# Kernel tuning notes

Measured on AMD Instinct MI355X. Metric: run time of the kernel, lower is better.

## Reference

```python
import jax, jax.numpy as jnp
import numpy as np

EPS = 1e-5

def conv2d(x, w, b=None, pad=1):
    # x: [B,C,H,W], w: [O,I,kh,kw]
    y = jax.lax.conv_general_dilated(x, w, (1, 1), [(pad, pad), (pad, pad)],
                                     dimension_numbers=('NCHW', 'OIHW', 'NCHW'))
    if b is not None:
        y = y + b[None, :, None, None]
    return y

def bn(x, g, b, m, v):
    # inference-mode batchnorm
    inv = g / jnp.sqrt(v + EPS)
    return x * inv[None, :, None, None] + (b - m * inv)[None, :, None, None]

def coord_conv(x, w, b):
    B, C, H, W = x.shape
    yy = jnp.broadcast_to(jnp.linspace(-1.0, 1.0, H)[:, None], (H, W))
    xx = jnp.broadcast_to(jnp.linspace(-1.0, 1.0, W)[None, :], (H, W))
    coords = jnp.broadcast_to(jnp.stack([xx, yy])[None], (B, 2, H, W)).astype(x.dtype)
    return conv2d(jnp.concatenate([x, coords], axis=1), w, b, pad=1)

def deform_conv(x, offset, w):
    # deformable conv v1, 3x3, pad=1, stride=1, no bias
    B, C, H, W = x.shape
    K = 9
    # offset channels interleaved (y, x) per kernel tap
    off = offset.reshape(B, K, 2, H, W)
    off_y, off_x = off[:, :, 0], off[:, :, 1]          # [B,9,H,W]
    k = jnp.arange(K)
    ko_y = (k // 3 - 1).astype(x.dtype)[None, :, None, None]
    ko_x = (k % 3 - 1).astype(x.dtype)[None, :, None, None]
    base_y = jnp.arange(H, dtype=x.dtype)[None, None, :, None]
    base_x = jnp.arange(W, dtype=x.dtype)[None, None, None, :]
    py = base_y + ko_y + off_y                          # [B,9,H,W]
    px = base_x + ko_x + off_x
    xf = x.reshape(B, C, H * W)
    y0 = jnp.floor(py)
    x0 = jnp.floor(px)
    acc = jnp.zeros((B, C, K, H, W), x.dtype)
    for dy in (0.0, 1.0):
        for dx in (0.0, 1.0):
            yy = y0 + dy
            xx = x0 + dx
            wgt = (1.0 - jnp.abs(py - yy)) * (1.0 - jnp.abs(px - xx))
            valid = (yy >= 0) & (yy < H) & (xx >= 0) & (xx < W)
            wgt = jnp.where(valid, wgt, 0.0)            # zero padding OOB
            yi = jnp.clip(yy, 0, H - 1).astype(jnp.int32)
            xi = jnp.clip(xx, 0, W - 1).astype(jnp.int32)
            idx = (yi * W + xi).reshape(B, K * H * W)
            v = jnp.take_along_axis(xf, idx[:, None, :], axis=2).reshape(B, C, K, H, W)
            acc = acc + v * wgt[:, None]
    wk = w.reshape(w.shape[0], w.shape[1], K)           # [O,I,9]
    return jnp.einsum('bckhw,ock->bohw', acc, wk)

def setup_inputs() -> dict:
    key = jax.random.key(0)
    ks = jax.random.split(key, 16)
    d_model, hd = 256, 64
    B, H, W = 8, 96, 96
    f32 = jnp.float32
    def bn_params(k):
        k1, k2, k3 = jax.random.split(k, 3)
        return (1.0 + 0.1 * jax.random.normal(k1, (hd,), f32),
                0.1 * jax.random.normal(k2, (hd,), f32),
                0.1 * jax.random.normal(k3, (hd,), f32),
                0.5 + jax.random.uniform(jax.random.fold_in(k, 7), (hd,), f32))
    bn1 = bn_params(ks[1]); bn2 = bn_params(ks[2]); bn3 = bn_params(ks[3]); bn4 = bn_params(ks[4])
    inp = {
        'features': jax.random.normal(ks[0], (B, H, W, d_model), f32),
        'coord_w': 0.05 * jax.random.normal(ks[5], (hd, d_model + 2, 3, 3), f32),
        'coord_b': jnp.zeros((hd,), f32),
        'bn1_g': bn1[0], 'bn1_b': bn1[1], 'bn1_m': bn1[2], 'bn1_v': bn1[3],
        'off_w': 0.01 * jax.random.normal(ks[6], (18, hd, 3, 3), f32),
        'off_b': 0.01 * jax.random.normal(ks[7], (18,), f32),
        'dc_w': 0.05 * jax.random.normal(ks[8], (hd, hd, 3, 3), f32),
        'bn2_g': bn2[0], 'bn2_b': bn2[1], 'bn2_m': bn2[2], 'bn2_v': bn2[3],
        'r1_w': 0.05 * jax.random.normal(ks[9], (hd, hd, 3, 3), f32),
        'bn3_g': bn3[0], 'bn3_b': bn3[1], 'bn3_m': bn3[2], 'bn3_v': bn3[3],
        'r2_w': 0.05 * jax.random.normal(ks[10], (hd, hd, 3, 3), f32),
        'bn4_g': bn4[0], 'bn4_b': bn4[1], 'bn4_m': bn4[2], 'bn4_v': bn4[3],
        'out_w': 0.1 * jax.random.normal(ks[11], (1, hd, 1, 1), f32),
        'out_b': jnp.zeros((1,), f32),
    }
    return inp

def reference(features, coord_w, coord_b, bn1_g, bn1_b, bn1_m, bn1_v,
              off_w, off_b, dc_w, bn2_g, bn2_b, bn2_m, bn2_v,
              r1_w, bn3_g, bn3_b, bn3_m, bn3_v,
              r2_w, bn4_g, bn4_b, bn4_m, bn4_v, out_w, out_b):
    x = jnp.transpose(features, (0, 3, 1, 2))           # NHWC -> NCHW
    x = jax.nn.relu(bn(coord_conv(x, coord_w, coord_b), bn1_g, bn1_b, bn1_m, bn1_v))
    offset = conv2d(x, off_w, off_b, pad=1)
    x = deform_conv(x, offset, dc_w)
    x = jax.nn.relu(bn(x, bn2_g, bn2_b, bn2_m, bn2_v))
    x = jax.nn.relu(bn(conv2d(x, r1_w, None, pad=1), bn3_g, bn3_b, bn3_m, bn3_v))
    x = jax.nn.relu(bn(conv2d(x, r2_w, None, pad=1), bn4_g, bn4_b, bn4_m, bn4_v))
    return jax.nn.sigmoid(conv2d(x, out_w, out_b, pad=0))
```

## Files before the change

### kernel.cpp

```cpp
#include <hip/hip_runtime.h>


typedef unsigned short u16;
typedef unsigned int u32;
typedef __attribute__((ext_vector_type(8)))  short bf16x8;
typedef __attribute__((ext_vector_type(16))) float f32x16;

#define EPSBN 1e-5f

__device__ __forceinline__ u16 f2bf(float f) {
  u32 u = __builtin_bit_cast(u32, f);
  u32 r = u + 0x7FFFu + ((u >> 16) & 1u);
  return (u16)(r >> 16);
}
__device__ __forceinline__ u32 pk2(float a, float b) {
  return (u32)f2bf(a) | ((u32)f2bf(b) << 16);
}
__device__ __forceinline__ float lo2f(u32 w) { return __builtin_bit_cast(float, w << 16); }
__device__ __forceinline__ float hi2f(u32 w) { return __builtin_bit_cast(float, w & 0xFFFF0000u); }

#define N_WCF 147456
#define N_WCC 9216
#define N_WOF 18432
#define N_W64 36864
#define N_ALLW (N_WCF + N_WCC + N_WOF + 3*N_W64)

__global__ __launch_bounds__(256) void prep_kernel(
    const float* __restrict__ coord_w, const float* __restrict__ off_w,
    const float* __restrict__ dc_w, const float* __restrict__ r1_w,
    const float* __restrict__ r2_w,
    u16* __restrict__ wcf, u16* __restrict__ wcc, u16* __restrict__ wof,
    u16* __restrict__ wdf, u16* __restrict__ wr1, u16* __restrict__ wr2)
{
  int i = blockIdx.x * 256 + threadIdx.x;
  if (i >= N_ALLW) return;
  int d = i;
  if (d < N_WCF) {
    int j = d & 7, lane = (d >> 3) & 63, frag = d >> 9;
    int nt = frag & 1, h = (frag >> 1) & 3, tap = (frag >> 3) % 9, cc = (frag >> 3) / 9;
    int ic = cc * 64 + h * 16 + ((lane >> 5) << 3) + j;
    int oc = nt * 32 + (lane & 31);
    wcf[d] = f2bf(coord_w[((size_t)oc * 258 + ic) * 9 + tap]);
    return;
  }
  d -= N_WCF;
  if (d < N_WCC) {
    int j = d & 7, lane = (d >> 3) & 63, frag = d >> 9;
    int nt = frag & 1, tap = frag >> 1;
    int ic = 256 + ((lane >> 5) << 3) + j;
    int oc = nt * 32 + (lane & 31);
    wcc[d] = (ic < 258) ? f2bf(coord_w[((size_t)oc * 258 + ic) * 9 + tap]) : (u16)0;
    return;
  }
  d -= N_WCC;
  if (d < N_WOF) {
    int j = d & 7, lane = (d >> 3) & 63, frag = d >> 9;
    int h = frag & 3, tap = frag >> 2;
    int ic = h * 16 + ((lane >> 5) << 3) + j;
    int oc = lane & 31;
    wof[d] = (oc < 18) ? f2bf(off_w[((size_t)oc * 64 + ic) * 9 + tap]) : (u16)0;
    return;
  }
  d -= N_WOF;
  int seg = d / N_W64;
  int e = d - seg * N_W64;
  int j = e & 7, lane = (e >> 3) & 63, frag = e >> 9;
  int nt = frag & 1, h = (frag >> 1) & 3, tap = frag >> 3;
  int ic = h * 16 + ((lane >> 5) << 3) + j;
  int oc = nt * 32 + (lane & 31);
  const float* src = (seg == 0) ? dc_w : (seg == 1) ? r1_w : r2_w;
  u16* dst = (seg == 0) ? wdf : (seg == 1) ? wr1 : wr2;
  dst[e] = f2bf(src[((size_t)oc * 64 + ic) * 9 + tap]);
}

__global__ __launch_bounds__(512, 2) void coord_conv_kernel(
    const float* __restrict__ feat, const u16* __restrict__ wcf,
    const u16* __restrict__ wcc, const float* __restrict__ cb,
    const float* __restrict__ g, const float* __restrict__ bb,
    const float* __restrict__ m, const float* __restrict__ v,
    u16* __restrict__ x1b)
{
  __shared__ __align__(16) u16 tile[6 * 34 * 72];
  const int t = threadIdx.x;
  const int wv = t >> 6, lane = t & 63;
  const int l31 = lane & 31, l5 = lane >> 5;
  const int rp = wv & 1, ntw = (wv >> 1) & 1, kh = wv >> 2;
  const int x0 = blockIdx.x * 32, y0 = blockIdx.y * 4, b = blockIdx.z;

  f32x16 acc[2] = {};
  float4 pa[4], pb[4];
  bf16x8 wfr[18];

  auto issueF = [&](int cc) {
    #pragma unroll
    for (int r = 0; r < 4; ++r) {
      const int i = t + r * 512;
      const float4 z = {0.f, 0.f, 0.f, 0.f};
      pa[r] = z; pb[r] = z;
      if (i < 1632) {
        const int px = i >> 3, gg = i & 7;
        const int ly = px / 34, lx = px - ly * 34;
        const int gy = y0 + ly - 1, gx = x0 + lx - 1;
        if ((unsigned)gy < 96u && (unsigned)gx < 96u) {
          const float* p = feat + ((size_t)((b * 96 + gy) * 96 + gx)) * 256
                           + cc * 64 + gg * 8;
          pa[r] = *(const float4*)p;
          pb[r] = *(const float4*)(p + 4);
        }
      }
    }
  };
  auto commitF = [&]() {
    #pragma unroll
    for (int r = 0; r < 4; ++r) {
      const int i = t + r * 512;
      if (i < 1632) {
        const int px = i >> 3, gg = i & 7;
        uint4 o;
        o.x = pk2(pa[r].x, pa[r].y); o.y = pk2(pa[r].z, pa[r].w);
        o.z = pk2(pb[r].x, pb[r].y); o.w = pk2(pb[r].z, pb[r].w);
        *(uint4*)(tile + px * 72 + gg * 8) = o;
      }
    }
  };
  auto loadW = [&](int cc) {
    #pragma unroll
    for (int tap = 0; tap < 9; ++tap)
      #pragma unroll
      for (int hh = 0; hh < 2; ++hh) {
        const int h = kh * 2 + hh;
        wfr[tap * 2 + hh] = *(const bf16x8*)(wcf +
            ((size_t)((((cc * 9 + tap) * 4 + h) * 2) + ntw)) * 512 + lane * 8);
      }
  };

  issueF(0);
  loadW(0);
  for (int cc = 0; cc < 4; ++cc) {
    __syncthreads();
    commitF();
    __syncthreads();
    if (cc < 3) issueF(cc + 1);
    #pragma unroll
    for (int tap = 0; tap < 9; ++tap) {
      const int dy = tap / 3, dx = tap - dy * 3;
      #pragma unroll
      for (int hh = 0; hh < 2; ++hh) {
        const bf16x8 bfr = wfr[tap * 2 + hh];
        #pragma unroll
        for (int ai = 0; ai < 2; ++ai) {
          const bf16x8 afr = *(const bf16x8*)(tile +
              ((rp * 2 + ai + dy) * 34 + l31 + dx) * 72
              + (kh * 2 + hh) * 16 + l5 * 8);
          acc[ai] = __builtin_amdgcn_mfma_f32_32x32x16_bf16(afr, bfr, acc[ai],
                                                            0, 0, 0);
        }
      }
    }
    if (cc < 3) loadW(cc + 1);
  }

  bf16x8 wcr[9];
  if (kh == 0) {
    #pragma unroll
    for (int tap = 0; tap < 9; ++tap)
      wcr[tap] = *(const bf16x8*)(wcc + ((size_t)(tap * 2 + ntw)) * 512
                                  + lane * 8);
  }
  __syncthreads();
  for (int i = t; i < 408; i += 512) {
    const int px = i >> 1, gg = i & 1;
    const int ly = px / 34, lx = px - ly * 34;
    const int gy = y0 + ly - 1, gx = x0 + lx - 1;
    uint4 o = {0u, 0u, 0u, 0u};
    if (gg == 0 && (unsigned)gy < 96u && (unsigned)gx < 96u) {
      const float xx = -1.f + (2.f / 95.f) * (float)gx;
      const float yy = -1.f + (2.f / 95.f) * (float)gy;
      o.x = pk2(xx, yy);
    }
    *(uint4*)(tile + (ly * 34 + lx) * 72 + gg * 8) = o;
  }
  __syncthreads();
  if (kh == 0) {
    #pragma unroll
    for (int tap = 0; tap < 9; ++tap) {
      const int dy = tap / 3, dx = tap - dy * 3;
      #pragma unroll
      for (int ai = 0; ai < 2; ++ai) {
        const bf16x8 afr = *(const bf16x8*)(tile +
            ((rp * 2 + ai + dy) * 34 + l31 + dx) * 72 + l5 * 8);
        acc[ai] = __builtin_amdgcn_mfma_f32_32x32x16_bf16(afr, wcr[tap],
                                                          acc[ai], 0, 0, 0);
      }
    }
  }

  float* redk = (float*)tile;
  const int slot = wv & 3;
  #pragma unroll
  for (int ai = 0; ai < 2; ++ai) {
    __syncthreads();
    if (kh == 1) {
      #pragma unroll
      for (int r = 0; r < 16; ++r)
        redk[(r * 4 + slot) * 64 + lane] = acc[ai][r];
    }
    __syncthreads();
    if (kh == 0) {
      #pragma unroll
      for (int r = 0; r < 16; ++r)
        acc[ai][r] += redk[(r * 4 + slot) * 64 + lane];
    }
  }

  if (kh == 0) {
    const int oc = ntw * 32 + l31;
    const float inv = g[oc] * rsqrtf(v[oc] + EPSBN);
    const float sh = bb[oc] - m[oc] * inv + cb[oc] * inv;
    #pragma unroll
    for (int ai = 0; ai < 2; ++ai) {
      const int y = y0 + rp * 2 + ai;
      #pragma unroll
      for (int r = 0; r < 16; ++r) {
        const int xr = (r & 3) + 8 * (r >> 2) + 4 * l5;
        const float val = fmaxf(fmaf(acc[ai][r], inv, sh), 0.f);
        x1b[((size_t)((b * 96 + y) * 96 + x0 + xr)) * 64 + oc] = f2bf(val);
      }
    }
  }
}

__global__ __launch_bounds__(512, 2) void deform_fused_kernel(
    const u16* __restrict__ x1b, const u16* __restrict__ wof,
    const float* __restrict__ offb_bias, const u16* __restrict__ wdf,
    const float* __restrict__ g, const float* __restrict__ bb,
    const float* __restrict__ m, const float* __restrict__ v,
    u16* __restrict__ x2b)
{
  __shared__ __align__(16) u16 xt[180 * 72];
  __shared__ __align__(16) u16 s[2 * 128 * 72];
  __shared__ float offs[128 * 18];
  const int t = threadIdx.x;
  const int wv = t >> 6, lane = t & 63;
  const int l31 = lane & 31, l5 = lane >> 5;
  const int x0 = blockIdx.x * 16, y0 = blockIdx.y * 8, b = blockIdx.z;

  {
    uint4 pf[3];
    #pragma unroll
    for (int rr = 0; rr < 3; ++rr) {
      const int i = t + rr * 512;
      const uint4 z = {0u, 0u, 0u, 0u};
      pf[rr] = z;
      if (i < 1440) {
        const int px = i >> 3, part = i & 7;
        const int ly = px / 18, lx = px - ly * 18;
        const int gy = y0 + ly - 1, gx = x0 + lx - 1;
        if ((unsigned)gy < 96u && (unsigned)gx < 96u)
          pf[rr] = *(const uint4*)(x1b +
              (((size_t)((b * 96 + gy) * 96 + gx)) << 6) + part * 8);
      }
    }
    #pragma unroll
    for (int rr = 0; rr < 3; ++rr) {
      const int i = t + rr * 512;
      if (i < 1440) {
        const int px = i >> 3, part = i & 7;
        *(uint4*)(xt + px * 72 + part * 8) = pf[rr];
      }
    }
  }
  __syncthreads();

  {
    const int mt = wv & 3, kh = wv >> 2;
    bf16x8 wfr[18];
    #pragma unroll
    for (int tap = 0; tap < 9; ++tap)
      #pragma unroll
      for (int hh = 0; hh < 2; ++hh)
        wfr[tap * 2 + hh] = *(const bf16x8*)(wof +
            ((size_t)(tap * 4 + kh * 2 + hh)) * 512 + lane * 8);
    const int px = mt * 32 + l31;
    const int r = px >> 4, c = px & 15;
    f32x16 acc = {};
    #pragma unroll
    for (int tap = 0; tap < 9; ++tap) {
      const int dy = tap / 3, dx = tap - dy * 3;
      #pragma unroll
      for (int hh = 0; hh < 2; ++hh) {
        const bf16x8 a = *(const bf16x8*)(xt +
            ((r + dy) * 18 + c + dx) * 72 + (kh * 2 + hh) * 16 + l5 * 8);
        acc = __builtin_amdgcn_mfma_f32_32x32x16_bf16(a, wfr[tap * 2 + hh],
                                                      acc, 0, 0, 0);
      }
    }
    float* redk = (float*)s;
    if (kh == 1) {
      #pragma unroll
      for (int r2 = 0; r2 < 16; ++r2)
        redk[(mt * 16 + r2) * 64 + lane] = acc[r2];
    }
    __syncthreads();
    if (kh == 0) {
      #pragma unroll
      for (int r2 = 0; r2 < 16; ++r2)
        acc[r2] += redk[(mt * 16 + r2) * 64 + lane];
      if (l31 < 18) {
        const float bs = offb_bias[l31];
        #pragma unroll
        for (int r2 = 0; r2 < 16; ++r2) {
          const int opx = mt * 32 + (r2 & 3) + 8 * (r2 >> 2) + 4 * l5;
          offs[opx * 18 + l31] = acc[r2] + bs;
        }
      }
    }
  }
  __syncthreads();

  const int mt = wv & 3, ntw = wv >> 2;
  const int sp = t >> 2, part = t & 3;
  const int sy = y0 + (sp >> 4), sx = x0 + (sp & 15);

  uint4 gbuf[8];
  float w4[4];

  auto prefetch = [&](int k) {
    const float oy = offs[sp * 18 + 2 * k];
    const float ox = offs[sp * 18 + 2 * k + 1];
    const float py = (float)(sy + k / 3 - 1) + oy;
    const float px = (float)(sx + k % 3 - 1) + ox;
    const float yf = floorf(py), xf = floorf(px);
    const float fy = py - yf, fx = px - xf;
    const int yi = (int)yf, xi = (int)xf;
    #pragma unroll
    for (int cor = 0; cor < 4; ++cor) {
      const int cy = yi + (cor >> 1), cx = xi + (cor & 1);
      const uint4 z = {0u, 0u, 0u, 0u};
      gbuf[2 * cor] = z; gbuf[2 * cor + 1] = z;
      const float wy = (cor & 2) ? fy : 1.f - fy;
      const float wx = (cor & 1) ? fx : 1.f - fx;
      w4[cor] = 0.f;
      if ((unsigned)cy < 96u && (unsigned)cx < 96u) {
        w4[cor] = wy * wx;
        const u16* p = x1b + ((size_t)((b * 96 + cy) * 96 + cx)) * 64
                       + part * 16;
        gbuf[2 * cor]     = *(const uint4*)p;
        gbuf[2 * cor + 1] = *(const uint4*)(p + 8);
      }
    }
  };
  auto combine = [&](u16* dst) {
    float val[16];
    #pragma unroll
    for (int j = 0; j < 16; ++j) val[j] = 0.f;
    #pragma unroll
    for (int cor = 0; cor < 4; ++cor) {
      const float wgt = w4[cor];
      const u32 uu[8] = {gbuf[2 * cor].x, gbuf[2 * cor].y,
                         gbuf[2 * cor].z, gbuf[2 * cor].w,
                         gbuf[2 * cor + 1].x, gbuf[2 * cor + 1].y,
                         gbuf[2 * cor + 1].z, gbuf[2 * cor + 1].w};
      #pragma unroll
      for (int u = 0; u < 8; ++u) {
        val[2 * u]     = fmaf(wgt, lo2f(uu[u]), val[2 * u]);
        val[2 * u + 1] = fmaf(wgt, hi2f(uu[u]), val[2 * u + 1]);
      }
    }
    u32 pk[8];
    #pragma unroll
    for (int u = 0; u < 8; ++u) pk[u] = pk2(val[2 * u], val[2 * u + 1]);
    uint4 w0 = {pk[0], pk[1], pk[2], pk[3]};
    uint4 w1 = {pk[4], pk[5], pk[6], pk[7]};
    *(uint4*)(dst + sp * 72 + part * 16) = w0;
    *(uint4*)(dst + sp * 72 + part * 16 + 8) = w1;
  };

  f32x16 acc = {};

  prefetch(0);
  combine(s);
  __syncthreads();

  for (int k = 0; k < 9; ++k) {
    u16* cur = s + (k & 1) * 9216;
    if (k < 8) prefetch(k + 1);
    #pragma unroll
    for (int h = 0; h < 4; ++h) {
      const bf16x8 afr = *(const bf16x8*)(cur + (mt * 32 + l31) * 72
                                          + h * 16 + l5 * 8);
      const bf16x8 bfr = *(const bf16x8*)(wdf +
          ((size_t)((k * 4 + h) * 2 + ntw)) * 512 + lane * 8);
      acc = __builtin_amdgcn_mfma_f32_32x32x16_bf16(afr, bfr, acc, 0, 0, 0);
    }
    if (k < 8) combine(s + ((k + 1) & 1) * 9216);
    __syncthreads();
  }

  const int oc = ntw * 32 + l31;
  const float inv = g[oc] * rsqrtf(v[oc] + EPSBN);
  const float sh = bb[oc] - m[oc] * inv;
  #pragma unroll
  for (int r = 0; r < 16; ++r) {
    const int pxi = mt * 32 + (r & 3) + 8 * (r >> 2) + 4 * l5;
    const int y = y0 + (pxi >> 4), x = x0 + (pxi & 15);
    const float val = fmaxf(fmaf(acc[r], inv, sh), 0.f);
    x2b[((size_t)((b * 96 + y) * 96 + x)) * 64 + oc] = f2bf(val);
  }
}

__global__ __launch_bounds__(512, 2) void tail_fused_kernel(
    const u16* __restrict__ x2b, const u16* __restrict__ wr1,
    const u16* __restrict__ wr2,
    const float* __restrict__ g3, const float* __restrict__ b3,
    const float* __restrict__ m3, const float* __restrict__ v3,
    const float* __restrict__ g4, const float* __restrict__ b4,
    const float* __restrict__ m4, const float* __restrict__ v4,
    const float* __restrict__ ow, const float* __restrict__ ob,
    float* __restrict__ outp)
{
  __shared__ __align__(16) u16 xt2[288 * 72];
  __shared__ __align__(16) u16 xt3[204 * 72];
  __shared__ float red2[2][128];
  const int t = threadIdx.x;
  const int wv = t >> 6, lane = t & 63;
  const int l31 = lane & 31, l5 = lane >> 5;
  const int x0 = blockIdx.x * 32, y0 = blockIdx.y * 4, b = blockIdx.z;

  {
    uint4 pf[5];
    #pragma unroll
    for (int rr = 0; rr < 5; ++rr) {
      const int i = t + rr * 512;
      const uint4 z = {0u, 0u, 0u, 0u};
      pf[rr] = z;
      if (i < 2304) {
        const int px = i >> 3, part = i & 7;
        const int ly = px / 36, lx = px - ly * 36;
        const int gy = y0 + ly - 2, gx = x0 + lx - 2;
        if ((unsigned)gy < 96u && (unsigned)gx < 96u)
          pf[rr] = *(const uint4*)(x2b +
              (((size_t)((b * 96 + gy) * 96 + gx)) << 6) + part * 8);
      }
    }
    #pragma unroll
    for (int rr = 0; rr < 5; ++rr) {
      const int i = t + rr * 512;
      if (i < 2304) {
        const int px = i >> 3, part = i & 7;
        *(uint4*)(xt2 + px * 72 + part * 8) = pf[rr];
      }
    }
  }
  __syncthreads();

  {
    const int nt = wv & 1, ms = wv >> 1;
    const int m1 = ms + 4;
    const bool has1 = (m1 < 7);
    const int pxc0 = min(ms * 32 + l31, 203);
    const int ly0 = pxc0 / 34, lx0 = pxc0 - ly0 * 34;
    const int pxc1 = min(m1 * 32 + l31, 203);
    const int ly1 = pxc1 / 34, lx1 = pxc1 - ly1 * 34;
    f32x16 a0 = {}, a1 = {};
    #pragma unroll
    for (int tap = 0; tap < 9; ++tap) {
      const int dy = tap / 3, dx = tap - dy * 3;
      #pragma unroll
      for (int h = 0; h < 4; ++h) {
        const bf16x8 wf = *(const bf16x8*)(wr1 +
            ((size_t)((tap * 4 + h) * 2 + nt)) * 512 + lane * 8);
        const bf16x8 f0 = *(const bf16x8*)(xt2 +
            ((ly0 + dy) * 36 + lx0 + dx) * 72 + h * 16 + l5 * 8);
        a0 = __builtin_amdgcn_mfma_f32_32x32x16_bf16(f0, wf, a0, 0, 0, 0);
        if (has1) {
          const bf16x8 f1 = *(const bf16x8*)(xt2 +
              ((ly1 + dy) * 36 + lx1 + dx) * 72 + h * 16 + l5 * 8);
          a1 = __builtin_amdgcn_mfma_f32_32x32x16_bf16(f1, wf, a1, 0, 0, 0);
        }
      }
    }
    const int oc = nt * 32 + l31;
    const float inv = g3[oc] * rsqrtf(v3[oc] + EPSBN);
    const float sh = b3[oc] - m3[oc] * inv;
    #pragma unroll
    for (int r = 0; r < 16; ++r) {
      const int xr = (r & 3) + 8 * (r >> 2) + 4 * l5;
      const int p0 = ms * 32 + xr;
      if (p0 < 204) {
        const int ly = p0 / 34, lx = p0 - ly * 34;
        const int gy = y0 + ly - 1, gx = x0 + lx - 1;
        const bool in0 = ((unsigned)gy < 96u) && ((unsigned)gx < 96u);
        xt3[p0 * 72 + oc] =
            in0 ? f2bf(fmaxf(fmaf(a0[r], inv, sh), 0.f)) : (u16)0;
      }
      if (has1) {
        const int p1 = m1 * 32 + xr;
        if (p1 < 204) {
          const int ly = p1 / 34, lx = p1 - ly * 34;
          const int gy = y0 + ly - 1, gx = x0 + lx - 1;
          const bool in1 = ((unsigned)gy < 96u) && ((unsigned)gx < 96u);
          xt3[p1 * 72 + oc] =
              in1 ? f2bf(fmaxf(fmaf(a1[r], inv, sh), 0.f)) : (u16)0;
        }
      }
    }
  }
  __syncthreads();

  {
    const int rp = wv & 1, ntw = (wv >> 1) & 1, kh = wv >> 2;
    bf16x8 wfr[18];
    #pragma unroll
    for (int tap = 0; tap < 9; ++tap)
      #pragma unroll
      for (int hh = 0; hh < 2; ++hh)
        wfr[tap * 2 + hh] = *(const bf16x8*)(wr2 +
            ((size_t)((tap * 4 + kh * 2 + hh) * 2 + ntw)) * 512 + lane * 8);
    f32x16 acc[2] = {};
    #pragma unroll
    for (int tap = 0; tap < 9; ++tap) {
      const int dy = tap / 3, dx = tap - dy * 3;
      #pragma unroll
      for (int hh = 0; hh < 2; ++hh) {
        const bf16x8 bfr = wfr[tap * 2 + hh];
        #pragma unroll
        for (int ai = 0; ai < 2; ++ai) {
          const bf16x8 a = *(const bf16x8*)(xt3 +
              ((rp * 2 + ai + dy) * 34 + l31 + dx) * 72
              + (kh * 2 + hh) * 16 + l5 * 8);
          acc[ai] = __builtin_amdgcn_mfma_f32_32x32x16_bf16(a, bfr, acc[ai],
                                                            0, 0, 0);
        }
      }
    }
    float* redk = (float*)xt2;
    __syncthreads();
    if (kh == 1) {
      #pragma unroll
      for (int ai = 0; ai < 2; ++ai)
        #pragma unroll
        for (int r = 0; r < 16; ++r)
          redk[(((rp * 2 + ai) * 2 + ntw) * 16 + r) * 64 + lane] = acc[ai][r];
    }
    __syncthreads();
    if (kh == 0) {
      const int oc = ntw * 32 + l31;
      const float inv = g4[oc] * rsqrtf(v4[oc] + EPSBN);
      const float sh = b4[oc] - m4[oc] * inv;
      const float wo = ow[oc];
      #pragma unroll
      for (int ai = 0; ai < 2; ++ai) {
        float pr[16];
        #pragma unroll
        for (int r = 0; r < 16; ++r) {
          const float a = acc[ai][r] +
              redk[(((rp * 2 + ai) * 2 + ntw) * 16 + r) * 64 + lane];
          const float val = fmaxf(fmaf(a, inv, sh), 0.f);
          pr[r] = val * wo;
        }
        #pragma unroll
        for (int mask = 1; mask <= 16; mask <<= 1)
          #pragma unroll
          for (int r = 0; r < 16; ++r)
            pr[r] += __shfl_xor(pr[r], mask);
        if (l31 == 0) {
          #pragma unroll
          for (int r = 0; r < 16; ++r) {
            const int xr = (r & 3) + 8 * (r >> 2) + 4 * l5;
            red2[ntw][(rp * 2 + ai) * 32 + xr] = pr[r];
          }
        }
      }
    }
    __syncthreads();
    if (t < 128) {
      const int yy = y0 + (t >> 5), xx = x0 + (t & 31);
      const float val = red2[0][t] + red2[1][t] + ob[0];
      outp[(size_t)(b * 96 + yy) * 96 + xx] = 1.f / (1.f + expf(-val));
    }
  }
}

extern "C" void kernel_launch(void* const* d_in, const int* in_sizes, int n_in,
                              void* d_out, int out_size, void* d_ws,
                              size_t ws_size, hipStream_t stream)
{
  (void)in_sizes; (void)n_in; (void)out_size; (void)ws_size;
  const float* features = (const float*)d_in[0];
  const float* coord_w  = (const float*)d_in[1];
  const float* coord_b  = (const float*)d_in[2];
  const float* bn1g = (const float*)d_in[3];
  const float* bn1b = (const float*)d_in[4];
  const float* bn1m = (const float*)d_in[5];
  const float* bn1v = (const float*)d_in[6];
  const float* off_w = (const float*)d_in[7];
  const float* off_b = (const float*)d_in[8];
  const float* dc_w  = (const float*)d_in[9];
  const float* bn2g = (const float*)d_in[10];
  const float* bn2b = (const float*)d_in[11];
  const float* bn2m = (const float*)d_in[12];
  const float* bn2v = (const float*)d_in[13];
  const float* r1_w = (const float*)d_in[14];
  const float* bn3g = (const float*)d_in[15];
  const float* bn3b = (const float*)d_in[16];
  const float* bn3m = (const float*)d_in[17];
  const float* bn3v = (const float*)d_in[18];
  const float* r2_w = (const float*)d_in[19];
  const float* bn4g = (const float*)d_in[20];
  const float* bn4b = (const float*)d_in[21];
  const float* bn4m = (const float*)d_in[22];
  const float* bn4v = (const float*)d_in[23];
  const float* out_w = (const float*)d_in[24];
  const float* out_b = (const float*)d_in[25];

  char* W = (char*)d_ws;
  u16* x1b = (u16*)W;
  u16* x2b = (u16*)(W + 9437184);
  u16* wcf = (u16*)(W + 18874368);
  u16* wcc = wcf + N_WCF;
  u16* wof = wcc + N_WCC;
  u16* wdf = wof + N_WOF;
  u16* wr1 = wdf + N_W64;
  u16* wr2 = wr1 + N_W64;

  prep_kernel<<<(N_ALLW + 255) / 256, 256, 0, stream>>>(
      coord_w, off_w, dc_w, r1_w, r2_w, wcf, wcc, wof, wdf, wr1, wr2);

  dim3 grid(3, 24, 8);
  dim3 gridD(6, 12, 8);

  coord_conv_kernel<<<grid, 512, 0, stream>>>(
      features, wcf, wcc, coord_b, bn1g, bn1b, bn1m, bn1v, x1b);
  deform_fused_kernel<<<gridD, 512, 0, stream>>>(
      x1b, wof, off_b, wdf, bn2g, bn2b, bn2m, bn2v, x2b);
  tail_fused_kernel<<<grid, 512, 0, stream>>>(
      x2b, wr1, wr2, bn3g, bn3b, bn3m, bn3v,
      bn4g, bn4b, bn4m, bn4v, out_w, out_b, (float*)d_out);
}
```

Measured before the change: 258.2 us.

## Serve deformable bilinear gathers from a wider LDS halo tile instead of global

```diff
diff --git a/kernel.cpp b/kernel.cpp
--- a/kernel.cpp
+++ b/kernel.cpp
@@ -237,8 +237,8 @@
     const float* __restrict__ m, const float* __restrict__ v,
     u16* __restrict__ x2b)
 {
-  __shared__ __align__(16) u16 xt[180 * 72];
-  __shared__ __align__(16) u16 s[2 * 128 * 72];
+  __shared__ __align__(16) u16 xt[240 * 72];
+  __shared__ __align__(16) u16 s[128 * 72];
   __shared__ float offs[128 * 18];
   const int t = threadIdx.x;
   const int wv = t >> 6, lane = t & 63;
@@ -246,25 +246,25 @@
   const int x0 = blockIdx.x * 16, y0 = blockIdx.y * 8, b = blockIdx.z;
 
   {
-    uint4 pf[3];
-    #pragma unroll
-    for (int rr = 0; rr < 3; ++rr) {
+    uint4 pf[4];
+    #pragma unroll
+    for (int rr = 0; rr < 4; ++rr) {
       const int i = t + rr * 512;
       const uint4 z = {0u, 0u, 0u, 0u};
       pf[rr] = z;
-      if (i < 1440) {
+      if (i < 1920) {
         const int px = i >> 3, part = i & 7;
-        const int ly = px / 18, lx = px - ly * 18;
-        const int gy = y0 + ly - 1, gx = x0 + lx - 1;
+        const int ly = px / 20, lx = px - ly * 20;
+        const int gy = y0 + ly - 2, gx = x0 + lx - 2;
         if ((unsigned)gy < 96u && (unsigned)gx < 96u)
           pf[rr] = *(const uint4*)(x1b +
               (((size_t)((b * 96 + gy) * 96 + gx)) << 6) + part * 8);
       }
     }
     #pragma unroll
-    for (int rr = 0; rr < 3; ++rr) {
+    for (int rr = 0; rr < 4; ++rr) {
       const int i = t + rr * 512;
-      if (i < 1440) {
+      if (i < 1920) {
         const int px = i >> 3, part = i & 7;
         *(uint4*)(xt + px * 72 + part * 8) = pf[rr];
       }
@@ -290,7 +290,8 @@
       #pragma unroll
       for (int hh = 0; hh < 2; ++hh) {
         const bf16x8 a = *(const bf16x8*)(xt +
-            ((r + dy) * 18 + c + dx) * 72 + (kh * 2 + hh) * 16 + l5 * 8);
+            ((r + 1 + dy) * 20 + (c + 1 + dx)) * 72
+            + (kh * 2 + hh) * 16 + l5 * 8);
         acc = __builtin_amdgcn_mfma_f32_32x32x16_bf16(a, wfr[tap * 2 + hh],
                                                       acc, 0, 0, 0);
       }
@@ -322,78 +323,64 @@
   const int sp = t >> 2, part = t & 3;
   const int sy = y0 + (sp >> 4), sx = x0 + (sp & 15);
 
-  uint4 gbuf[8];
-  float w4[4];
-
-  auto prefetch = [&](int k) {
-    const float oy = offs[sp * 18 + 2 * k];
-    const float ox = offs[sp * 18 + 2 * k + 1];
-    const float py = (float)(sy + k / 3 - 1) + oy;
-    const float px = (float)(sx + k % 3 - 1) + ox;
-    const float yf = floorf(py), xf = floorf(px);
-    const float fy = py - yf, fx = px - xf;
-    const int yi = (int)yf, xi = (int)xf;
-    #pragma unroll
-    for (int cor = 0; cor < 4; ++cor) {
-      const int cy = yi + (cor >> 1), cx = xi + (cor & 1);
-      const uint4 z = {0u, 0u, 0u, 0u};
-      gbuf[2 * cor] = z; gbuf[2 * cor + 1] = z;
-      const float wy = (cor & 2) ? fy : 1.f - fy;
-      const float wx = (cor & 1) ? fx : 1.f - fx;
-      w4[cor] = 0.f;
-      if ((unsigned)cy < 96u && (unsigned)cx < 96u) {
-        w4[cor] = wy * wx;
-        const u16* p = x1b + ((size_t)((b * 96 + cy) * 96 + cx)) * 64
-                       + part * 16;
-        gbuf[2 * cor]     = *(const uint4*)p;
-        gbuf[2 * cor + 1] = *(const uint4*)(p + 8);
-      }
-    }
-  };
-  auto combine = [&](u16* dst) {
-    float val[16];
-    #pragma unroll
-    for (int j = 0; j < 16; ++j) val[j] = 0.f;
-    #pragma unroll
-    for (int cor = 0; cor < 4; ++cor) {
-      const float wgt = w4[cor];
-      const u32 uu[8] = {gbuf[2 * cor].x, gbuf[2 * cor].y,
-                         gbuf[2 * cor].z, gbuf[2 * cor].w,
-                         gbuf[2 * cor + 1].x, gbuf[2 * cor + 1].y,
-                         gbuf[2 * cor + 1].z, gbuf[2 * cor + 1].w};
-      #pragma unroll
-      for (int u = 0; u < 8; ++u) {
-        val[2 * u]     = fmaf(wgt, lo2f(uu[u]), val[2 * u]);
-        val[2 * u + 1] = fmaf(wgt, hi2f(uu[u]), val[2 * u + 1]);
-      }
-    }
-    u32 pk[8];
-    #pragma unroll
-    for (int u = 0; u < 8; ++u) pk[u] = pk2(val[2 * u], val[2 * u + 1]);
-    uint4 w0 = {pk[0], pk[1], pk[2], pk[3]};
-    uint4 w1 = {pk[4], pk[5], pk[6], pk[7]};
-    *(uint4*)(dst + sp * 72 + part * 16) = w0;
-    *(uint4*)(dst + sp * 72 + part * 16 + 8) = w1;
-  };
-
   f32x16 acc = {};
 
-  prefetch(0);
-  combine(s);
-  __syncthreads();
-
   for (int k = 0; k < 9; ++k) {
-    u16* cur = s + (k & 1) * 9216;
-    if (k < 8) prefetch(k + 1);
+    {
+      const float oy = offs[sp * 18 + 2 * k];
+      const float ox = offs[sp * 18 + 2 * k + 1];
+      const float py = (float)(sy + k / 3 - 1) + oy;
+      const float px = (float)(sx + k % 3 - 1) + ox;
+      const float yf = floorf(py), xf = floorf(px);
+      const float fy = py - yf, fx = px - xf;
+      const int yi = (int)yf, xi = (int)xf;
+      float val[16];
+      #pragma unroll
+      for (int j = 0; j < 16; ++j) val[j] = 0.f;
+      #pragma unroll
+      for (int cor = 0; cor < 4; ++cor) {
+        const int cy = yi + (cor >> 1), cx = xi + (cor & 1);
+        if ((unsigned)cy < 96u && (unsigned)cx < 96u) {
+          const float wy = (cor & 2) ? fy : 1.f - fy;
+          const float wx = (cor & 1) ? fx : 1.f - fx;
+          const float wgt = wy * wx;
+          const int ty = cy - y0 + 2, tx = cx - x0 + 2;
+          uint4 ua, ub;
+          if ((unsigned)ty < 12u && (unsigned)tx < 20u) {
+            const u16* p = xt + (ty * 20 + tx) * 72 + part * 16;
+            ua = *(const uint4*)p;
+            ub = *(const uint4*)(p + 8);
+          } else {
+            const u16* p = x1b + ((size_t)((b * 96 + cy) * 96 + cx)) * 64
+                           + part * 16;
+            ua = *(const uint4*)p;
+            ub = *(const uint4*)(p + 8);
+          }
+          const u32 uu[8] = {ua.x, ua.y, ua.z, ua.w, ub.x, ub.y, ub.z, ub.w};
+          #pragma unroll
+          for (int u = 0; u < 8; ++u) {
+            val[2 * u]     = fmaf(wgt, lo2f(uu[u]), val[2 * u]);
+            val[2 * u + 1] = fmaf(wgt, hi2f(uu[u]), val[2 * u + 1]);
+          }
+        }
+      }
+      u32 pk[8];
+      #pragma unroll
+      for (int u = 0; u < 8; ++u) pk[u] = pk2(val[2 * u], val[2 * u + 1]);
+      uint4 w0 = {pk[0], pk[1], pk[2], pk[3]};
+      uint4 w1 = {pk[4], pk[5], pk[6], pk[7]};
+      *(uint4*)(s + sp * 72 + part * 16) = w0;
+      *(uint4*)(s + sp * 72 + part * 16 + 8) = w1;
+    }
+    __syncthreads();
     #pragma unroll
     for (int h = 0; h < 4; ++h) {
-      const bf16x8 afr = *(const bf16x8*)(cur + (mt * 32 + l31) * 72
+      const bf16x8 afr = *(const bf16x8*)(s + (mt * 32 + l31) * 72
                                           + h * 16 + l5 * 8);
       const bf16x8 bfr = *(const bf16x8*)(wdf +
           ((size_t)((k * 4 + h) * 2 + ntw)) * 512 + lane * 8);
       acc = __builtin_amdgcn_mfma_f32_32x32x16_bf16(afr, bfr, acc, 0, 0, 0);
     }
-    if (k < 8) combine(s + ((k + 1) & 1) * 9216);
     __syncthreads();
   }
 
```

Result: no change. 256.6 us (-0.6%).
